# Performance work log

Measured on AMD Instinct MI355X. Metric: run time of the kernel, lower is better.

Reference implementation:

```python
import jax, jax.numpy as jnp
import numpy as np

D_IN = 1024
D_OUT = 1024
SEQ = 4096


def setup_inputs() -> dict:
    key = jax.random.key(0)
    kx, kq, kk, kv = jax.random.split(key, 4)
    x = jax.random.normal(kx, (SEQ, D_IN), dtype=jnp.float32)
    # original uses torch.rand (uniform [0,1)) for parameter init
    w_query = jax.random.uniform(kq, (D_IN, D_OUT), dtype=jnp.float32)
    w_key = jax.random.uniform(kk, (D_IN, D_OUT), dtype=jnp.float32)
    w_value = jax.random.uniform(kv, (D_IN, D_OUT), dtype=jnp.float32)
    return {"x": x, "w_query": w_query, "w_key": w_key, "w_value": w_value}


def reference(x, w_query, w_key, w_value):
    # QKV projections: [S, d_in] @ [d_in, d_out] -> [S, d_out]
    queries = x @ w_query
    keys = x @ w_key
    values = x @ w_value
    scale = keys.shape[-1] ** 0.5
    # full attention matrix [S, S]
    attn_scores = jnp.einsum('sd,td->st', queries, keys)
    attn_weights = jax.nn.softmax(attn_scores / scale, axis=-1)
    context_vecs = attn_weights @ values  # [S, d_out]
    return context_vecs
```

## Files before the change

### kernel.cpp

```cpp
#include <hip/hip_runtime.h>
#include <hip/hip_fp16.h>
#include <math.h>

#define SEQ    4096
#define DMODEL 1024

typedef _Float16 half8   __attribute__((ext_vector_type(8)));
typedef _Float16 half4v  __attribute__((ext_vector_type(4)));
typedef float    floatx4 __attribute__((ext_vector_type(4)));

__device__ inline void split_val(float v, _Float16& h, _Float16& l) {
    _Float16 hh = (_Float16)v;
    h = hh;
    l = (_Float16)(v - (float)hh);
}

__global__ __launch_bounds__(256) void prep(const float* __restrict__ x,
                                            const float* __restrict__ wq,
                                            const float* __restrict__ wk,
                                            const float* __restrict__ wv,
                                            _Float16* __restrict__ x_hi,
                                            _Float16* __restrict__ x_lo,
                                            _Float16* __restrict__ wqkT_hi,
                                            _Float16* __restrict__ wqkT_lo,
                                            _Float16* __restrict__ wvT) {
    __shared__ float tile[32][33];
    const int b = blockIdx.x;
    if (b < 3072) {
        const int which = b >> 10;
        const int bb = b & 1023;
        const int c0 = (bb & 31) * 32;
        const int r0 = (bb >> 5) * 32;
        const float* w = (which == 0) ? wq : (which == 1) ? wk : wv;
        const int tx = threadIdx.x & 31, ty = threadIdx.x >> 5;
#pragma unroll
        for (int j = 0; j < 4; ++j)
            tile[ty * 4 + j][tx] = w[(size_t)(r0 + ty * 4 + j) * DMODEL + c0 + tx];
        __syncthreads();
        if (which < 2) {
            _Float16* th = wqkT_hi + (size_t)which * DMODEL * DMODEL;
            _Float16* tl = wqkT_lo + (size_t)which * DMODEL * DMODEL;
#pragma unroll
            for (int j = 0; j < 4; ++j) {
                float v = tile[tx][ty * 4 + j];
                size_t idx = (size_t)(c0 + ty * 4 + j) * DMODEL + r0 + tx;
                _Float16 h, l;
                split_val(v, h, l);
                th[idx] = h;
                tl[idx] = l;
            }
        } else {
#pragma unroll
            for (int j = 0; j < 4; ++j)
                wvT[(size_t)(c0 + ty * 4 + j) * DMODEL + r0 + tx] =
                    (_Float16)tile[tx][ty * 4 + j];
        }
    } else {
        const int t0 = (b - 3072) * 256 + threadIdx.x;
#pragma unroll
        for (int rep = 0; rep < 4; ++rep) {
            const size_t i = (size_t)t0 + (size_t)rep * 262144;
            floatx4 v = *(const floatx4*)(x + 4 * i);
            half4v h, l;
#pragma unroll
            for (int j = 0; j < 4; ++j) {
                _Float16 hh = (_Float16)v[j];
                _Float16 ll = (_Float16)(v[j] - (float)hh);
                h[j] = hh;
                l[j] = ll;
            }
            *(half4v*)(x_hi + 4 * i) = h;
            *(half4v*)(x_lo + 4 * i) = l;
        }
    }
}

__global__ __launch_bounds__(512, 1) void gemm_qkproj_dp(
    const _Float16* __restrict__ Ahi, const _Float16* __restrict__ Alo,
    const _Float16* __restrict__ Bhi, const _Float16* __restrict__ Blo,
    _Float16* __restrict__ Qcat, _Float16* __restrict__ Kcat) {
    __shared__ _Float16 As[4][128][32];
    __shared__ _Float16 Bs[4][256][32];

    const int tid  = threadIdx.x;
    const int lane = tid & 63;
    const int wid  = tid >> 6;
    const int wm   = (wid >> 2) * 64;
    const int wn   = (wid & 3) * 64;

    const int rowA0 = blockIdx.y * 128;
    const int colB0 = blockIdx.x * 256;

    const int ar  = tid >> 2;
    const int ag  = tid & 3;
    const int ags = ag ^ ((ar >> 1) & 3);
    const char* aHiB = (const char*)(Ahi + (size_t)(rowA0 + ar) * DMODEL) + ags * 16;
    const char* aLoB = (const char*)(Alo + (size_t)(rowA0 + ar) * DMODEL) + ags * 16;
    const int br  = tid >> 2;
    const int bg  = tid & 3;
    const int bgs = bg ^ ((br >> 1) & 3);
    const char* bHi0 = (const char*)(Bhi + (size_t)(colB0 + br) * DMODEL) + bgs * 16;
    const char* bHi1 = (const char*)(Bhi + (size_t)(colB0 + br + 128) * DMODEL) + bgs * 16;
    const char* bLo0 = (const char*)(Blo + (size_t)(colB0 + br) * DMODEL) + bgs * 16;
    const char* bLo1 = (const char*)(Blo + (size_t)(colB0 + br + 128) * DMODEL) + bgs * 16;

#define STAGE_QA(tt)                                                                 \
    do {                                                                             \
        const int _s = (tt) & 3;                                                     \
        const char* _ab = ((tt) < 64) ? aHiB : aLoB;                                 \
        const size_t _ko = (size_t)((tt) & 31) * 64;                                 \
        __builtin_amdgcn_global_load_lds(                                            \
            (const __attribute__((address_space(1))) void*)(_ab + _ko),              \
            (__attribute__((address_space(3))) void*)&As[_s][ar][ag * 8], 16, 0, 0); \
    } while (0)

#define STAGE_QB(tt)                                                                 \
    do {                                                                             \
        const int _s = (tt) & 3;                                                     \
        const bool _lo = ((tt) >= 32) && ((tt) < 64);                                \
        const char* _b0 = _lo ? bLo0 : bHi0;                                         \
        const char* _b1 = _lo ? bLo1 : bHi1;                                         \
        const size_t _ko = (size_t)((tt) & 31) * 64;                                 \
        __builtin_amdgcn_global_load_lds(                                            \
            (const __attribute__((address_space(1))) void*)(_b0 + _ko),              \
            (__attribute__((address_space(3))) void*)&Bs[_s][br][bg * 8], 16, 0, 0); \
        __builtin_amdgcn_global_load_lds(                                            \
            (const __attribute__((address_space(1))) void*)(_b1 + _ko),              \
            (__attribute__((address_space(3))) void*)&Bs[_s][br + 128][bg * 8], 16, 0, 0);\
    } while (0)

    const int fm = lane & 15;
    const int fq = lane >> 4;
    const int ck = (fq ^ ((fm >> 1) & 3)) * 8;

    floatx4 acc[4][4] = {};

    auto tile_body = [&](int t, bool do_stage) {
        const int s = t & 3;
        half8 av[4], bv[4];
#pragma unroll
        for (int i = 0; i < 4; ++i) av[i] = *(const half8*)&As[s][wm + i * 16 + fm][ck];
#pragma unroll
        for (int j = 0; j < 4; ++j) bv[j] = *(const half8*)&Bs[s][wn + j * 16 + fm][ck];
        if (do_stage) { STAGE_QA(t + 3); STAGE_QB(t + 3); }
        asm volatile("" ::: "memory");
        __builtin_amdgcn_s_barrier();
        asm volatile("" ::: "memory");
        __builtin_amdgcn_s_setprio(1);
#pragma unroll
        for (int i = 0; i < 4; ++i)
#pragma unroll
            for (int j = 0; j < 4; ++j)
                acc[i][j] = __builtin_amdgcn_mfma_f32_16x16x32_f16(av[i], bv[j], acc[i][j], 0, 0, 0);
        __builtin_amdgcn_s_setprio(0);
    };

    STAGE_QA(0); STAGE_QB(0);
    STAGE_QA(1); STAGE_QB(1);
    STAGE_QA(2); STAGE_QB(2);
    asm volatile("s_waitcnt vmcnt(6)" ::: "memory");
    __builtin_amdgcn_s_barrier();
    asm volatile("" ::: "memory");

#pragma unroll 1
    for (int t = 0; t < 93; ++t) {
        tile_body(t, true);
        asm volatile("s_waitcnt vmcnt(6)" ::: "memory");
        __builtin_amdgcn_s_barrier();
        asm volatile("" ::: "memory");
    }
    tile_body(93, false);
    asm volatile("s_waitcnt vmcnt(3)" ::: "memory");
    __builtin_amdgcn_s_barrier();
    asm volatile("" ::: "memory");
    tile_body(94, false);
    asm volatile("s_waitcnt vmcnt(0)" ::: "memory");
    __builtin_amdgcn_s_barrier();
    asm volatile("" ::: "memory");
    tile_body(95, false);
#undef STAGE_QA
#undef STAGE_QB

    _Float16* dcat = Qcat;
    int cbase = colB0;
    if (colB0 >= 1024) { dcat = Kcat; cbase = colB0 - 1024; }

#pragma unroll
    for (int i = 0; i < 4; ++i) {
        const int growb = rowA0 + wm + i * 16 + fq * 4;
#pragma unroll
        for (int j = 0; j < 4; ++j) {
            const int gcol = wn + j * 16 + fm;
#pragma unroll
            for (int r = 0; r < 4; ++r) {
                float v = acc[i][j][r];
                size_t idx = (size_t)(growb + r) * 2048 + cbase + gcol;
                _Float16 h, l;
                split_val(v, h, l);
                dcat[idx] = h;
                dcat[idx + 1024] = l;
            }
        }
    }
}

__global__ __launch_bounds__(512, 2) void gemm_score_dp(
    const _Float16* __restrict__ Qc,
    const _Float16* __restrict__ Kc,
    _Float16* __restrict__ Ph, float* __restrict__ Marr, float* __restrict__ Larr,
    float scale) {
    __shared__ _Float16 As[4][256][32];
    __shared__ _Float16 Bs[4][256][32];

    const int tid  = threadIdx.x;
    const int lane = tid & 63;
    const int wid  = tid >> 6;
    const int wm   = (wid >> 2) * 128;
    const int wn   = (wid & 3) * 64;

    const int lin = blockIdx.y * 16 + blockIdx.x;
    const int swz = (lin & 7) * 32 + (lin >> 3);
    const int rowA0 = (swz >> 4) * 256;
    const int colB0 = (swz & 15) * 256;

    const int pr  = tid >> 2;
    const int pg  = tid & 3;
    const int pgs = pg ^ ((pr >> 1) & 3);

    const char* aSrc0 = (const char*)(Qc + (size_t)(rowA0 + pr) * 2048) + pgs * 16;
    const char* aSrc1 = (const char*)(Qc + (size_t)(rowA0 + pr + 128) * 2048) + pgs * 16;
    const char* bSrc0 = (const char*)(Kc + (size_t)(colB0 + pr) * 2048) + pgs * 16;
    const char* bSrc1 = (const char*)(Kc + (size_t)(colB0 + pr + 128) * 2048) + pgs * 16;

#define STAGE_A(t)                                                                  \
    do {                                                                            \
        const int _s = (t) & 3;                                                     \
        const size_t _ko = (size_t)(t) * 64;                                        \
        __builtin_amdgcn_global_load_lds(                                           \
            (const __attribute__((address_space(1))) void*)(aSrc0 + _ko),           \
            (__attribute__((address_space(3))) void*)&As[_s][pr][pg * 8], 16, 0, 0);\
        __builtin_amdgcn_global_load_lds(                                           \
            (const __attribute__((address_space(1))) void*)(aSrc1 + _ko),           \
            (__attribute__((address_space(3))) void*)&As[_s][pr + 128][pg * 8], 16, 0, 0);\
    } while (0)

#define STAGE_B(t)                                                                  \
    do {                                                                            \
        const int _s = (t) & 3;                                                     \
        const size_t _ko = (size_t)(t) * 64;                                        \
        __builtin_amdgcn_global_load_lds(                                           \
            (const __attribute__((address_space(1))) void*)(bSrc0 + _ko),           \
            (__attribute__((address_space(3))) void*)&Bs[_s][pr][pg * 8], 16, 0, 0);\
        __builtin_amdgcn_global_load_lds(                                           \
            (const __attribute__((address_space(1))) void*)(bSrc1 + _ko),           \
            (__attribute__((address_space(3))) void*)&Bs[_s][pr + 128][pg * 8], 16, 0, 0);\
    } while (0)

    const int fm = lane & 15;
    const int fq = lane >> 4;
    const int ck = (fq ^ ((fm >> 1) & 3)) * 8;

    floatx4 acc[8][4] = {};

    auto tile_body = [&](int t, bool do_stage) {
        const int s = t & 3;
        half8 av[4], av2[4], bv[4];
#pragma unroll
        for (int i = 0; i < 4; ++i) av[i]  = *(const half8*)&As[s][wm + i * 16 + fm][ck];
#pragma unroll
        for (int i = 0; i < 4; ++i) av2[i] = *(const half8*)&As[s][wm + 64 + i * 16 + fm][ck];
#pragma unroll
        for (int j = 0; j < 4; ++j) bv[j]  = *(const half8*)&Bs[s][wn + j * 16 + fm][ck];
        if (do_stage) { STAGE_A(t + 3); STAGE_B(t + 3); }
        asm volatile("" ::: "memory");
        __builtin_amdgcn_s_barrier();
        asm volatile("" ::: "memory");
        __builtin_amdgcn_s_setprio(1);
#pragma unroll
        for (int i = 0; i < 4; ++i)
#pragma unroll
            for (int j = 0; j < 4; ++j)
                acc[i][j] = __builtin_amdgcn_mfma_f32_16x16x32_f16(av[i], bv[j], acc[i][j], 0, 0, 0);
#pragma unroll
        for (int i = 0; i < 4; ++i)
#pragma unroll
            for (int j = 0; j < 4; ++j)
                acc[i + 4][j] = __builtin_amdgcn_mfma_f32_16x16x32_f16(av2[i], bv[j], acc[i + 4][j], 0, 0, 0);
        __builtin_amdgcn_s_setprio(0);
    };

    STAGE_A(0); STAGE_B(0);
    STAGE_A(1); STAGE_B(1);
    STAGE_A(2); STAGE_B(2);
    asm volatile("s_waitcnt vmcnt(8)" ::: "memory");
    __builtin_amdgcn_s_barrier();
    asm volatile("" ::: "memory");

#pragma unroll 1
    for (int t = 0; t < 61; ++t) {
        tile_body(t, true);
        asm volatile("s_waitcnt vmcnt(8)" ::: "memory");
        __builtin_amdgcn_s_barrier();
        asm volatile("" ::: "memory");
    }
    tile_body(61, false);
    asm volatile("s_waitcnt vmcnt(4)" ::: "memory");
    __builtin_amdgcn_s_barrier();
    asm volatile("" ::: "memory");
    tile_body(62, false);
    asm volatile("s_waitcnt vmcnt(0)" ::: "memory");
    __builtin_amdgcn_s_barrier();
    asm volatile("" ::: "memory");
    tile_body(63, false);
#undef STAGE_A
#undef STAGE_B

    const int tprime = (colB0 + wn) >> 6;
#pragma unroll
    for (int i = 0; i < 8; ++i) {
#pragma unroll
        for (int r = 0; r < 4; ++r) {
            const int grow = rowA0 + wm + i * 16 + fq * 4 + r;
            float s0 = acc[i][0][r] * scale;
            float s1 = acc[i][1][r] * scale;
            float s2 = acc[i][2][r] * scale;
            float s3 = acc[i][3][r] * scale;
            float mx = fmaxf(fmaxf(s0, s1), fmaxf(s2, s3));
            mx = fmaxf(mx, __shfl_xor(mx, 1));
            mx = fmaxf(mx, __shfl_xor(mx, 2));
            mx = fmaxf(mx, __shfl_xor(mx, 4));
            mx = fmaxf(mx, __shfl_xor(mx, 8));
            float p0 = __expf(s0 - mx);
            float p1 = __expf(s1 - mx);
            float p2 = __expf(s2 - mx);
            float p3 = __expf(s3 - mx);
            float sum = p0 + p1 + p2 + p3;
            sum += __shfl_xor(sum, 1);
            sum += __shfl_xor(sum, 2);
            sum += __shfl_xor(sum, 4);
            sum += __shfl_xor(sum, 8);
            _Float16* prow = Ph + (size_t)grow * SEQ + colB0 + wn + fm;
            prow[0]  = (_Float16)p0;
            prow[16] = (_Float16)p1;
            prow[32] = (_Float16)p2;
            prow[48] = (_Float16)p3;
            if (fm == 0) {
                Marr[(size_t)grow * 64 + tprime] = mx;
                Larr[(size_t)grow * 64 + tprime] = sum;
            }
        }
    }
}

__global__ __launch_bounds__(256) void compute_c(const float* __restrict__ Marr,
                                                 const float* __restrict__ Larr,
                                                 _Float16* __restrict__ CarrT) {
    __shared__ float c_s[64][65];
    const int row0 = blockIdx.x * 64;
    const int wv = threadIdx.x >> 6;
    const int ln = threadIdx.x & 63;

#pragma unroll
    for (int k = 0; k < 16; ++k) {
        const int r = wv * 16 + k;
        float mt = Marr[(size_t)(row0 + r) * 64 + ln];
        float lt = Larr[(size_t)(row0 + r) * 64 + ln];
        float m = mt;
#pragma unroll
        for (int off = 32; off > 0; off >>= 1) m = fmaxf(m, __shfl_xor(m, off));
        float e = __expf(mt - m);
        float L = lt * e;
#pragma unroll
        for (int off = 32; off > 0; off >>= 1) L += __shfl_xor(L, off);
        c_s[r][ln] = e / L;
    }
    __syncthreads();

#pragma unroll
    for (int k = 0; k < 16; ++k) {
        const int t = wv * 16 + k;
        CarrT[(size_t)t * SEQ + row0 + ln] = (_Float16)c_s[ln][t];
    }
}

__global__ __launch_bounds__(512, 1) void gemm_pv_dp(
    const _Float16* __restrict__ P,
    const _Float16* __restrict__ VT,
    const _Float16* __restrict__ CarrT,
    float* __restrict__ out) {
    __shared__ _Float16 As[4][128][64];
    __shared__ _Float16 Bs[4][128][64];
    __shared__ _Float16 cT[64][128];

    const int tid  = threadIdx.x;
    const int lane = tid & 63;
    const int wid  = tid >> 6;
    const int wm   = (wid >> 2) * 64;
    const int wn   = (wid & 3) * 32;

    const int rowA0 = blockIdx.y * 128;
    const int colB0 = blockIdx.x * 128;

    {
        int g = tid;
#pragma unroll
        for (int it = 0; it < 2; ++it, g += 512) {
            const int t  = g >> 4;
            const int r8 = (g & 15) * 8;
            *(half8*)&cT[t][r8] =
                *(const half8*)(CarrT + (size_t)t * SEQ + rowA0 + r8);
        }
    }
    __syncthreads();

    const int prow = tid >> 3;
    const int pgr  = tid & 7;
    const int ags  = pgr ^ (prow & 7);
    const char* aSrc0 = (const char*)(P  + (size_t)(rowA0 + prow) * SEQ) + ags * 16;
    const char* aSrc1 = (const char*)(P  + (size_t)(rowA0 + prow + 64) * SEQ) + ags * 16;
    const char* bSrc0 = (const char*)(VT + (size_t)(colB0 + prow) * SEQ) + ags * 16;
    const char* bSrc1 = (const char*)(VT + (size_t)(colB0 + prow + 64) * SEQ) + ags * 16;

#define STAGE_PA(tt)                                                                \
    do {                                                                            \
        const int _s = (tt) & 3;                                                    \
        const size_t _ko = (size_t)(tt) * 128;                                      \
        __builtin_amdgcn_global_load_lds(                                           \
            (const __attribute__((address_space(1))) void*)(aSrc0 + _ko),           \
            (__attribute__((address_space(3))) void*)&As[_s][prow][pgr * 8], 16, 0, 0);\
        __builtin_amdgcn_global_load_lds(                                           \
            (const __attribute__((address_space(1))) void*)(aSrc1 + _ko),           \
            (__attribute__((address_space(3))) void*)&As[_s][prow + 64][pgr * 8], 16, 0, 0);\
    } while (0)

#define STAGE_PB(tt)                                                                \
    do {                                                                            \
        const int _s = (tt) & 3;                                                    \
        const size_t _ko = (size_t)(tt) * 128;                                      \
        __builtin_amdgcn_global_load_lds(                                           \
            (const __attribute__((address_space(1))) void*)(bSrc0 + _ko),           \
            (__attribute__((address_space(3))) void*)&Bs[_s][prow][pgr * 8], 16, 0, 0);\
        __builtin_amdgcn_global_load_lds(                                           \
            (const __attribute__((address_space(1))) void*)(bSrc1 + _ko),           \
            (__attribute__((address_space(3))) void*)&Bs[_s][prow + 64][pgr * 8], 16, 0, 0);\
    } while (0)

    const int fm = lane & 15;
    const int fq = lane >> 4;
    const int ck0 = ((fq    ) ^ (fm & 7)) * 8;
    const int ck1 = ((fq + 4) ^ (fm & 7)) * 8;

    floatx4 acc[4][2] = {};

    auto tile_body = [&](int t, bool do_stage) {
        const int s = t & 3;
        half8 av[4], av2[4], bv[2], bv2[2];
        _Float16 cs[4];
#pragma unroll
        for (int i = 0; i < 4; ++i) {
            av[i]  = *(const half8*)&As[s][wm + i * 16 + fm][ck0];
            av2[i] = *(const half8*)&As[s][wm + i * 16 + fm][ck1];
            cs[i]  = cT[t][wm + i * 16 + fm];
        }
#pragma unroll
        for (int j = 0; j < 2; ++j) {
            bv[j]  = *(const half8*)&Bs[s][wn + j * 16 + fm][ck0];
            bv2[j] = *(const half8*)&Bs[s][wn + j * 16 + fm][ck1];
        }
#pragma unroll
        for (int i = 0; i < 4; ++i)
#pragma unroll
            for (int e = 0; e < 8; ++e) {
                av[i][e]  *= cs[i];
                av2[i][e] *= cs[i];
            }
        if (do_stage) { STAGE_PA(t + 3); STAGE_PB(t + 3); }
        asm volatile("" ::: "memory");
        __builtin_amdgcn_s_barrier();
        asm volatile("" ::: "memory");
        __builtin_amdgcn_s_setprio(1);
#pragma unroll
        for (int i = 0; i < 4; ++i)
#pragma unroll
            for (int j = 0; j < 2; ++j)
                acc[i][j] = __builtin_amdgcn_mfma_f32_16x16x32_f16(av[i], bv[j], acc[i][j], 0, 0, 0);
#pragma unroll
        for (int i = 0; i < 4; ++i)
#pragma unroll
            for (int j = 0; j < 2; ++j)
                acc[i][j] = __builtin_amdgcn_mfma_f32_16x16x32_f16(av2[i], bv2[j], acc[i][j], 0, 0, 0);
        __builtin_amdgcn_s_setprio(0);
    };

    STAGE_PA(0); STAGE_PB(0);
    STAGE_PA(1); STAGE_PB(1);
    STAGE_PA(2); STAGE_PB(2);
    asm volatile("s_waitcnt vmcnt(8)" ::: "memory");
    __builtin_amdgcn_s_barrier();
    asm volatile("" ::: "memory");

#pragma unroll 1
    for (int t = 0; t < 61; ++t) {
        tile_body(t, true);
        asm volatile("s_waitcnt vmcnt(8)" ::: "memory");
        __builtin_amdgcn_s_barrier();
        asm volatile("" ::: "memory");
    }
    tile_body(61, false);
    asm volatile("s_waitcnt vmcnt(4)" ::: "memory");
    __builtin_amdgcn_s_barrier();
    asm volatile("" ::: "memory");
    tile_body(62, false);
    asm volatile("s_waitcnt vmcnt(0)" ::: "memory");
    __builtin_amdgcn_s_barrier();
    asm volatile("" ::: "memory");
    tile_body(63, false);
#undef STAGE_PA
#undef STAGE_PB

#pragma unroll
    for (int i = 0; i < 4; ++i) {
        const int growb = rowA0 + wm + i * 16 + fq * 4;
#pragma unroll
        for (int j = 0; j < 2; ++j) {
            const int gcol = colB0 + wn + j * 16 + fm;
#pragma unroll
            for (int r = 0; r < 4; ++r)
                out[(size_t)(growb + r) * DMODEL + gcol] = acc[i][j][r];
        }
    }
}

template <int OUT_HALF>
__global__ __launch_bounds__(256) void gemm_h16_n64(
    const _Float16* __restrict__ A, int lda,
    const _Float16* __restrict__ B, int ldb,
    float* __restrict__ Cf, _Float16* __restrict__ Ch,
    int N, int K) {
    __shared__ _Float16 Ah[128][32];
    __shared__ _Float16 Bh[64][32];

    const int tid = threadIdx.x;
    const int lane = tid & 63;
    const int w = tid >> 6;
    const int wm = (w >> 1) * 64;
    const int wn = (w & 1) * 32;

    const int rowA0 = blockIdx.y * 128;
    const int colB0 = blockIdx.x * 64;

    const int sr = lane >> 2;
    const int sc = lane & 3;
    const int ra0 = w * 32 + sr;
    const int ra1 = ra0 + 16;
    const int rb0 = w * 16 + sr;
    const int cga0 = sc ^ ((ra0 >> 1) & 3);
    const int cga1 = sc ^ ((ra1 >> 1) & 3);
    const int cgb0 = sc ^ ((rb0 >> 1) & 3);

    const char* gp[3];
    gp[0] = (const char*)(A + (size_t)(rowA0 + ra0) * lda) + cga0 * 16;
    gp[1] = (const char*)(A + (size_t)(rowA0 + ra1) * lda) + cga1 * 16;
    gp[2] = (const char*)(B + (size_t)(colB0 + rb0) * ldb) + cgb0 * 16;

    _Float16* lp[3] = {
        &Ah[w * 32][0], &Ah[w * 32 + 16][0],
        &Bh[w * 16][0],
    };

    const int fm = lane & 15;
    const int fq = lane >> 4;
    const int ck = ((fq ^ ((fm >> 1) & 3)) * 8);

    floatx4 acc[4][2] = {};

    for (int k0 = 0; k0 < K; k0 += 32) {
#pragma unroll
        for (int t = 0; t < 3; ++t)
            __builtin_amdgcn_global_load_lds(
                (const __attribute__((address_space(1))) void*)gp[t],
                (__attribute__((address_space(3))) void*)lp[t], 16, 0, 0);
#pragma unroll
        for (int t = 0; t < 3; ++t) gp[t] += 64;
        __syncthreads();

        half8 av[4], bv[2];
#pragma unroll
        for (int i = 0; i < 4; ++i)
            av[i] = *(const half8*)&Ah[wm + i * 16 + fm][ck];
#pragma unroll
        for (int j = 0; j < 2; ++j)
            bv[j] = *(const half8*)&Bh[wn + j * 16 + fm][ck];
#pragma unroll
        for (int i = 0; i < 4; ++i)
#pragma unroll
            for (int j = 0; j < 2; ++j)
                acc[i][j] = __builtin_amdgcn_mfma_f32_16x16x32_f16(av[i], bv[j], acc[i][j], 0, 0, 0);
        __syncthreads();
    }

#pragma unroll
    for (int i = 0; i < 4; ++i) {
        const int growb = rowA0 + wm + i * 16 + fq * 4;
#pragma unroll
        for (int j = 0; j < 2; ++j) {
            const int gcol = colB0 + wn + j * 16 + fm;
#pragma unroll
            for (int r = 0; r < 4; ++r) {
                float v = acc[i][j][r];
                size_t idx = (size_t)(growb + r) * N + gcol;
                if (OUT_HALF) Ch[idx] = (_Float16)v;
                else          Cf[idx] = v;
            }
        }
    }
}

extern "C" void kernel_launch(void* const* d_in, const int* in_sizes, int n_in,
                              void* d_out, int out_size, void* d_ws, size_t ws_size,
                              hipStream_t stream) {
    const float* x  = (const float*)d_in[0];
    const float* wq = (const float*)d_in[1];
    const float* wk = (const float*)d_in[2];
    const float* wv = (const float*)d_in[3];
    float* out = (float*)d_out;

    char* base = (char*)d_ws;
    const size_t MB = 1u << 20;
    _Float16* P       = (_Float16*)base;
    _Float16* x_hi    = (_Float16*)(base + 0 * MB);
    _Float16* x_lo    = (_Float16*)(base + 8 * MB);
    _Float16* wqkT_hi = (_Float16*)(base + 16 * MB);
    _Float16* wqkT_lo = (_Float16*)(base + 20 * MB);
    _Float16* wvT     = (_Float16*)(base + 24 * MB);
    float*    Marr    = (float*)(base + 32 * MB);
    float*    Larr    = (float*)(base + 33 * MB);
    _Float16* CarrT   = (_Float16*)(base + 34 * MB);
    _Float16* Qcat    = (_Float16*)(base + 64 * MB);
    _Float16* Kcat    = (_Float16*)(base + 80 * MB);
    _Float16* VT      = (_Float16*)(base + 96 * MB);

    prep<<<4096, 256, 0, stream>>>(x, wq, wk, wv, x_hi, x_lo, wqkT_hi, wqkT_lo, wvT);

    dim3 gqk(2048 / 256, SEQ / 128);
    gemm_qkproj_dp<<<gqk, dim3(512), 0, stream>>>(x_hi, x_lo, wqkT_hi, wqkT_lo,
                                                  Qcat, Kcat);
    dim3 gvt(SEQ / 64, DMODEL / 128);
    gemm_h16_n64<1><<<gvt, 256, 0, stream>>>(wvT, DMODEL, x_hi, DMODEL,
                                             nullptr, VT, SEQ, DMODEL);

    dim3 gs(SEQ / 256, SEQ / 256);
    gemm_score_dp<<<gs, dim3(512), 0, stream>>>(Qcat, Kcat, P, Marr, Larr,
                                                1.0f / 32.0f);

    compute_c<<<SEQ / 64, 256, 0, stream>>>(Marr, Larr, CarrT);

    dim3 gpv(DMODEL / 128, SEQ / 128);
    gemm_pv_dp<<<gpv, dim3(512), 0, stream>>>(P, VT, CarrT, out);
}
```

Baseline: 290.7 us.

## Drop mid-tile barrier and interleave LDS fragment reads with MFMA in GEMM loops

In all three pipelined GEMM kernels, each tile's prefetch of the stage three tiles ahead is now issued at the start of the tile. The barrier that used to sit between the LDS fragment reads and the MFMAs is removed, leaving one fence per tile. That fence drains LDS reads (lgkmcnt(0)) and the required global-to-LDS loads before the barrier, so the slot being overwritten is no longer being read. The second half of the fragment loads (av2/bv2 and the scaling) is moved after the first MFMA group so LDS latency overlaps matrix work. This halves block-wide synchronisation per tile, at the risk of extra register pressure or worse compiler scheduling around the sched_barrier.

Result: slower. 354.2 us (+21.9%).

```diff
diff --git a/kernel.cpp b/kernel.cpp
--- a/kernel.cpp
+++ b/kernel.cpp
@@ -75,6 +75,15 @@
     }
 }
 
+#define TILE_FENCE(N)                                             \
+    do {                                                          \
+        __builtin_amdgcn_sched_barrier(0);                        \
+        asm volatile("s_waitcnt lgkmcnt(0)" ::: "memory");        \
+        asm volatile("s_waitcnt vmcnt(" #N ")" ::: "memory");     \
+        __builtin_amdgcn_s_barrier();                             \
+        asm volatile("" ::: "memory");                            \
+    } while (0)
+
 __global__ __launch_bounds__(512, 1) void gemm_qkproj_dp(
     const _Float16* __restrict__ Ahi, const _Float16* __restrict__ Alo,
     const _Float16* __restrict__ Bhi, const _Float16* __restrict__ Blo,
@@ -137,16 +146,13 @@
 
     auto tile_body = [&](int t, bool do_stage) {
         const int s = t & 3;
+        if (do_stage) { STAGE_QA(t + 3); STAGE_QB(t + 3); }
+        __builtin_amdgcn_s_setprio(1);
         half8 av[4], bv[4];
 #pragma unroll
         for (int i = 0; i < 4; ++i) av[i] = *(const half8*)&As[s][wm + i * 16 + fm][ck];
 #pragma unroll
         for (int j = 0; j < 4; ++j) bv[j] = *(const half8*)&Bs[s][wn + j * 16 + fm][ck];
-        if (do_stage) { STAGE_QA(t + 3); STAGE_QB(t + 3); }
-        asm volatile("" ::: "memory");
-        __builtin_amdgcn_s_barrier();
-        asm volatile("" ::: "memory");
-        __builtin_amdgcn_s_setprio(1);
 #pragma unroll
         for (int i = 0; i < 4; ++i)
 #pragma unroll
@@ -165,18 +171,12 @@
 #pragma unroll 1
     for (int t = 0; t < 93; ++t) {
         tile_body(t, true);
-        asm volatile("s_waitcnt vmcnt(6)" ::: "memory");
-        __builtin_amdgcn_s_barrier();
-        asm volatile("" ::: "memory");
+        TILE_FENCE(6);
     }
     tile_body(93, false);
-    asm volatile("s_waitcnt vmcnt(3)" ::: "memory");
-    __builtin_amdgcn_s_barrier();
-    asm volatile("" ::: "memory");
+    TILE_FENCE(3);
     tile_body(94, false);
-    asm volatile("s_waitcnt vmcnt(0)" ::: "memory");
-    __builtin_amdgcn_s_barrier();
-    asm volatile("" ::: "memory");
+    TILE_FENCE(0);
     tile_body(95, false);
 #undef STAGE_QA
 #undef STAGE_QB
@@ -264,23 +264,20 @@
 
     auto tile_body = [&](int t, bool do_stage) {
         const int s = t & 3;
+        if (do_stage) { STAGE_A(t + 3); STAGE_B(t + 3); }
+        __builtin_amdgcn_s_setprio(1);
         half8 av[4], av2[4], bv[4];
 #pragma unroll
         for (int i = 0; i < 4; ++i) av[i]  = *(const half8*)&As[s][wm + i * 16 + fm][ck];
 #pragma unroll
-        for (int i = 0; i < 4; ++i) av2[i] = *(const half8*)&As[s][wm + 64 + i * 16 + fm][ck];
-#pragma unroll
         for (int j = 0; j < 4; ++j) bv[j]  = *(const half8*)&Bs[s][wn + j * 16 + fm][ck];
-        if (do_stage) { STAGE_A(t + 3); STAGE_B(t + 3); }
-        asm volatile("" ::: "memory");
-        __builtin_amdgcn_s_barrier();
-        asm volatile("" ::: "memory");
-        __builtin_amdgcn_s_setprio(1);
 #pragma unroll
         for (int i = 0; i < 4; ++i)
 #pragma unroll
             for (int j = 0; j < 4; ++j)
                 acc[i][j] = __builtin_amdgcn_mfma_f32_16x16x32_f16(av[i], bv[j], acc[i][j], 0, 0, 0);
+#pragma unroll
+        for (int i = 0; i < 4; ++i) av2[i] = *(const half8*)&As[s][wm + 64 + i * 16 + fm][ck];
 #pragma unroll
         for (int i = 0; i < 4; ++i)
 #pragma unroll
@@ -299,18 +296,12 @@
 #pragma unroll 1
     for (int t = 0; t < 61; ++t) {
         tile_body(t, true);
-        asm volatile("s_waitcnt vmcnt(8)" ::: "memory");
-        __builtin_amdgcn_s_barrier();
-        asm volatile("" ::: "memory");
+        TILE_FENCE(8);
     }
     tile_body(61, false);
-    asm volatile("s_waitcnt vmcnt(4)" ::: "memory");
-    __builtin_amdgcn_s_barrier();
-    asm volatile("" ::: "memory");
+    TILE_FENCE(4);
     tile_body(62, false);
-    asm volatile("s_waitcnt vmcnt(0)" ::: "memory");
-    __builtin_amdgcn_s_barrier();
-    asm volatile("" ::: "memory");
+    TILE_FENCE(0);
     tile_body(63, false);
 #undef STAGE_A
 #undef STAGE_B
@@ -454,36 +445,34 @@
 
     auto tile_body = [&](int t, bool do_stage) {
         const int s = t & 3;
+        if (do_stage) { STAGE_PA(t + 3); STAGE_PB(t + 3); }
+        __builtin_amdgcn_s_setprio(1);
         half8 av[4], av2[4], bv[2], bv2[2];
         _Float16 cs[4];
 #pragma unroll
         for (int i = 0; i < 4; ++i) {
             av[i]  = *(const half8*)&As[s][wm + i * 16 + fm][ck0];
-            av2[i] = *(const half8*)&As[s][wm + i * 16 + fm][ck1];
             cs[i]  = cT[t][wm + i * 16 + fm];
         }
 #pragma unroll
-        for (int j = 0; j < 2; ++j) {
-            bv[j]  = *(const half8*)&Bs[s][wn + j * 16 + fm][ck0];
-            bv2[j] = *(const half8*)&Bs[s][wn + j * 16 + fm][ck1];
-        }
-#pragma unroll
-        for (int i = 0; i < 4; ++i)
-#pragma unroll
-            for (int e = 0; e < 8; ++e) {
-                av[i][e]  *= cs[i];
-                av2[i][e] *= cs[i];
-            }
-        if (do_stage) { STAGE_PA(t + 3); STAGE_PB(t + 3); }
-        asm volatile("" ::: "memory");
-        __builtin_amdgcn_s_barrier();
-        asm volatile("" ::: "memory");
-        __builtin_amdgcn_s_setprio(1);
+        for (int j = 0; j < 2; ++j) bv[j] = *(const half8*)&Bs[s][wn + j * 16 + fm][ck0];
+#pragma unroll
+        for (int i = 0; i < 4; ++i)
+#pragma unroll
+            for (int e = 0; e < 8; ++e) av[i][e] *= cs[i];
 #pragma unroll
         for (int i = 0; i < 4; ++i)
 #pragma unroll
             for (int j = 0; j < 2; ++j)
                 acc[i][j] = __builtin_amdgcn_mfma_f32_16x16x32_f16(av[i], bv[j], acc[i][j], 0, 0, 0);
+#pragma unroll
+        for (int i = 0; i < 4; ++i) av2[i] = *(const half8*)&As[s][wm + i * 16 + fm][ck1];
+#pragma unroll
+        for (int j = 0; j < 2; ++j) bv2[j] = *(const half8*)&Bs[s][wn + j * 16 + fm][ck1];
+#pragma unroll
+        for (int i = 0; i < 4; ++i)
+#pragma unroll
+            for (int e = 0; e < 8; ++e) av2[i][e] *= cs[i];
 #pragma unroll
         for (int i = 0; i < 4; ++i)
 #pragma unroll
@@ -502,18 +491,12 @@
 #pragma unroll 1
     for (int t = 0; t < 61; ++t) {
         tile_body(t, true);
-        asm volatile("s_waitcnt vmcnt(8)" ::: "memory");
-        __builtin_amdgcn_s_barrier();
-        asm volatile("" ::: "memory");
+        TILE_FENCE(8);
     }
     tile_body(61, false);
-    asm volatile("s_waitcnt vmcnt(4)" ::: "memory");
-    __builtin_amdgcn_s_barrier();
-    asm volatile("" ::: "memory");
+    TILE_FENCE(4);
     tile_body(62, false);
-    asm volatile("s_waitcnt vmcnt(0)" ::: "memory");
-    __builtin_amdgcn_s_barrier();
-    asm volatile("" ::: "memory");
+    TILE_FENCE(0);
     tile_body(63, false);
 #undef STAGE_PA
 #undef STAGE_PB
```
